# Performance work log

Measured on AMD Instinct MI355X. Metric: run time of the kernel, lower is better.

Reference implementation:

```python
import jax, jax.numpy as jnp
import numpy as np

N_CONST = 188
P = 16
HIDDEN = 128
DE = 5
DO = 6
N_TARGETS = 5
BATCH = 32


def _edge_indices(n):
    # receiver/sender pairs in the same order as itertools.product, skipping diagonal
    r, s = np.meshgrid(np.arange(n), np.arange(n), indexing='ij')
    mask = r != s
    return jnp.asarray(r[mask]), jnp.asarray(s[mask])  # each [n*(n-1)]


def _linear_params(key, fan_in, fan_out):
    kw, kb = jax.random.split(key)
    w = jax.random.normal(kw, (fan_in, fan_out), jnp.float32) / np.sqrt(fan_in)
    b = jax.random.normal(kb, (fan_out,), jnp.float32) * 0.01
    return w, b


def setup_inputs() -> dict:
    key = jax.random.key(0)
    ks = jax.random.split(key, 10)
    inp = {"x": jax.random.normal(ks[0], (BATCH, N_CONST, P), jnp.float32)}
    h2 = HIDDEN // 2
    dims = [
        ("fr1", 2 * P, HIDDEN), ("fr2", HIDDEN, h2), ("fr3", h2, DE),
        ("fo1", P + DE, HIDDEN), ("fo2", HIDDEN, h2), ("fo3", h2, DO),
        ("fc1", DO * N_CONST, HIDDEN), ("fc2", HIDDEN, h2), ("fc3", h2, N_TARGETS),
    ]
    for i, (name, fi, fo) in enumerate(dims):
        w, b = _linear_params(ks[i + 1], fi, fo)
        inp[name + "_w"] = w
        inp[name + "_b"] = b
    return inp


def reference(x, fr1_w, fr1_b, fr2_w, fr2_b, fr3_w, fr3_b,
              fo1_w, fo1_b, fo2_w, fo2_b, fo3_w, fo3_b,
              fc1_w, fc1_b, fc2_w, fc2_b, fc3_w, fc3_b):
    B, n, p = x.shape
    recv, send = _edge_indices(n)  # [Nr]
    # gather receiver/sender node features (replaces one-hot matmuls with Rr, Rs)
    e_in = jnp.concatenate([x[:, recv], x[:, send]], axis=-1)  # [B, Nr, 2P]
    h = jax.nn.relu(e_in @ fr1_w + fr1_b)
    h = jax.nn.relu(h @ fr2_w + fr2_b)
    E = jax.nn.relu(h @ fr3_w + fr3_b)  # [B, Nr, De]
    # scatter-add edge effects back to receiver nodes (replaces E @ Rr^T)
    Ebar = jnp.zeros((B, n, E.shape[-1]), x.dtype).at[:, recv].add(E)  # [B, N, De]
    c = jnp.concatenate([x, Ebar], axis=-1)  # [B, N, P+De]
    h = jax.nn.relu(c @ fo1_w + fo1_b)
    h = jax.nn.relu(h @ fo2_w + fo2_b)
    O = jax.nn.relu(h @ fo3_w + fo3_b)  # [B, N, Do]
    h = jax.nn.relu(O.reshape(B, -1) @ fc1_w + fc1_b)
    h = jax.nn.relu(h @ fc2_w + fc2_b)
    return h @ fc3_w + fc3_b  # [B, n_targets]
```

## Files before the change

### kernel.cpp

```cpp
#include <hip/hip_runtime.h>

#define BB   32
#define NN   188
#define PP   16
#define HID  128
#define HH2  64
#define DE   5
#define DO   6
#define NT   5
#define ROWS_O (BB*NN)
#define RT   32
#define KO   (PP+DE)

typedef __attribute__((ext_vector_type(8))) short short8;
typedef __attribute__((ext_vector_type(4))) float float4_;
typedef __attribute__((ext_vector_type(4))) unsigned uint4_;

__device__ __forceinline__ short f2bf(float v) {
    union { float f; unsigned u; } a; a.f = v;
    unsigned r = a.u + 0x7fff + ((a.u >> 16) & 1);
    return (short)(r >> 16);
}
__device__ __forceinline__ unsigned r2u(float v) {
    v = v > 0.f ? v : 0.f;
    return __float_as_uint(v) + 0x8000u;
}
__device__ __forceinline__ unsigned pack_hi16(unsigned hi, unsigned lo) {
    return __builtin_amdgcn_perm(hi, lo, 0x07060302);
}

#define XB_OFF    0
#define XB_ELTS   (BB*NN*24)
#define W1T_OFF   (XB_OFF + XB_ELTS)
#define W1T_ELTS  (HID*40)
#define W2S_OFF   (W1T_OFF + W1T_ELTS)
#define W2S_ELTS  (16*64*8)
#define W3S_OFF   (W2S_OFF + W2S_ELTS)
#define W3S_ELTS  (2*64*8)
#define SHORT_TOTAL (W3S_OFF + W3S_ELTS)

__device__ __forceinline__ int kmap(int q, int e) {
    return (e < 4) ? (q*4 + e) : (16 + q*4 + (e - 4));
}

__global__ void prep_kernel(const float* __restrict__ x,
                            const float* __restrict__ w1,
                            const float* __restrict__ w2,
                            const float* __restrict__ w3,
                            short* __restrict__ ws)
{
    const int i = blockIdx.x * blockDim.x + threadIdx.x;
    const int stride = gridDim.x * blockDim.x;
    for (int idx = i; idx < BB*NN*PP; idx += stride) {
        int row = idx >> 4, k = idx & 15;
        ws[XB_OFF + row*24 + k] = f2bf(x[idx]);
    }
    for (int idx = i; idx < 32*HID; idx += stride) {
        int k = idx >> 7, n = idx & 127;
        ws[W1T_OFF + n*40 + k] = f2bf(w1[idx]);
    }
    for (int idx = i; idx < W2S_ELTS; idx += stride) {
        int f = idx >> 9;
        int l = (idx >> 3) & 63;
        int e = idx & 7;
        int tt = f >> 2, s = f & 3;
        int q = l >> 4, n16 = l & 15;
        int k = 32*s + kmap(q, e);
        int n = tt*16 + n16;
        ws[W2S_OFF + idx] = f2bf(w2[k*HH2 + n]);
    }
    for (int idx = i; idx < W3S_ELTS; idx += stride) {
        int s2 = idx >> 9;
        int l = (idx >> 3) & 63;
        int e = idx & 7;
        int q = l >> 4, n16 = l & 15;
        int k = 32*s2 + kmap(q, e);
        ws[W3S_OFF + idx] = (n16 < DE) ? f2bf(w3[k*DE + n16]) : (short)0;
    }
}

__global__ __launch_bounds__(256)
void edge_mfma_kernel(const short* __restrict__ ws_s,
                      const float* __restrict__ b1,
                      const float* __restrict__ b2,
                      const float* __restrict__ b3,
                      float* __restrict__ ebar)
{
    const short* xb  = ws_s + XB_OFF;
    const short* w1t = ws_s + W1T_OFF;
    const short* w3g = ws_s + W3S_OFF;

    __shared__ __align__(16) unsigned wsmem[4096];
    __shared__ __align__(16) float sB1[HID];

    const int tid  = threadIdx.x;
    const int wave = tid >> 6;
    const int lane = tid & 63;
    const int n16  = lane & 15;
    const int q    = lane >> 4;
    const int bi   = blockIdx.x * 4 + wave;
    const int b    = bi / NN;
    const int recv = bi - b*NN;

    {
        const uint4* src = (const uint4*)(ws_s + W2S_OFF);
        uint4* dst = (uint4*)wsmem;
        #pragma unroll
        for (int i = 0; i < 4; ++i) dst[tid + i*256] = src[tid + i*256];
    }
    if (tid < HID) sB1[tid] = b1[tid];

    short8 W1f[8];
    #pragma unroll
    for (int t = 0; t < 8; ++t)
        W1f[t] = *(const short8*)(w1t + (t*16 + n16)*40 + q*8);
    short8 W3f[2];
    #pragma unroll
    for (int s = 0; s < 2; ++s)
        W3f[s] = *(const short8*)(w3g + s*512 + lane*8);
    float4_ bias2v[4];
    #pragma unroll
    for (int tt = 0; tt < 4; ++tt)
        bias2v[tt] = *(const float4_*)(b2 + tt*16 + q*4);
    float4_ bias3r;
    #pragma unroll
    for (int rg = 0; rg < 4; ++rg) {
        int o = q*4 + rg;
        bias3r[rg] = (o < DE) ? b3[o] : 0.f;
    }

    __syncthreads();

    const short* w2l = (const short*)wsmem;
    const short* xrow = xb + b*(NN*24);
    const bool rside = (q < 2);

    float acc[4] = {0.f, 0.f, 0.f, 0.f};

    short8 E1;
    {
        int send0 = n16 + (n16 >= recv ? 1 : 0);
        const int node = rside ? recv : send0;
        E1 = *(const short8*)(xrow + node*24 + (q & 1)*8);
    }

    #pragma unroll 2
    for (int ti = 0; ti < 12; ++ti) {
        short8 E1c = E1;
        if (ti < 11) {
            int en = (ti+1)*16 + n16;
            int send = en + (en >= recv ? 1 : 0);
            if (send > NN-1) send = NN-1;
            const int node = rside ? recv : send;
            E1 = *(const short8*)(xrow + node*24 + (q & 1)*8);
        }

        float4_ C2[4];
        #pragma unroll
        for (int tt = 0; tt < 4; ++tt) C2[tt] = bias2v[tt];

        #pragma unroll
        for (int s = 0; s < 4; ++s) {
            float4_ cb0 = *(const float4_*)(sB1 + (2*s)*16   + q*4);
            float4_ cb1 = *(const float4_*)(sB1 + (2*s+1)*16 + q*4);
            float4_ Ca = __builtin_amdgcn_mfma_f32_16x16x32_bf16(W1f[2*s],   E1c, cb0, 0, 0, 0);
            float4_ Cb = __builtin_amdgcn_mfma_f32_16x16x32_bf16(W1f[2*s+1], E1c, cb1, 0, 0, 0);
            uint4_ dv = (uint4_){ pack_hi16(r2u(Ca[1]), r2u(Ca[0])),
                                  pack_hi16(r2u(Ca[3]), r2u(Ca[2])),
                                  pack_hi16(r2u(Cb[1]), r2u(Cb[0])),
                                  pack_hi16(r2u(Cb[3]), r2u(Cb[2])) };
            short8 Bf = __builtin_bit_cast(short8, dv);
            #pragma unroll
            for (int tt = 0; tt < 4; ++tt) {
                short8 A2 = *(const short8*)(w2l + (tt*4 + s)*512 + lane*8);
                C2[tt] = __builtin_amdgcn_mfma_f32_16x16x32_bf16(A2, Bf, C2[tt], 0, 0, 0);
            }
        }

        float4_ C3 = bias3r;
        #pragma unroll
        for (int s2 = 0; s2 < 2; ++s2) {
            float4_ Cc = C2[2*s2], Cd = C2[2*s2+1];
            uint4_ dv = (uint4_){ pack_hi16(r2u(Cc[1]), r2u(Cc[0])),
                                  pack_hi16(r2u(Cc[3]), r2u(Cc[2])),
                                  pack_hi16(r2u(Cd[1]), r2u(Cd[0])),
                                  pack_hi16(r2u(Cd[3]), r2u(Cd[2])) };
            short8 B3f = __builtin_bit_cast(short8, dv);
            C3 = __builtin_amdgcn_mfma_f32_16x16x32_bf16(W3f[s2], B3f, C3, 0, 0, 0);
        }
        const int e = ti*16 + n16;
        const bool ok = (e < NN-1);
        #pragma unroll
        for (int rg = 0; rg < 4; ++rg) {
            float v = C3[rg];
            v = v > 0.f ? v : 0.f;
            acc[rg] += ok ? v : 0.f;
        }
    }

    #pragma unroll
    for (int rg = 0; rg < 4; ++rg) {
        acc[rg] += __shfl_xor(acc[rg], 1);
        acc[rg] += __shfl_xor(acc[rg], 2);
        acc[rg] += __shfl_xor(acc[rg], 4);
        acc[rg] += __shfl_xor(acc[rg], 8);
    }
    if (n16 == 0) {
        #pragma unroll
        for (int rg = 0; rg < 4; ++rg) {
            int o = q*4 + rg;
            if (o < DE) ebar[bi*DE + o] = acc[rg];
        }
    }
}

__global__ __launch_bounds__(512)
void obj_mlp_kernel(const float* __restrict__ x, const float* __restrict__ ebar,
                    const float* __restrict__ w1, const float* __restrict__ b1,
                    const float* __restrict__ w2, const float* __restrict__ b2,
                    const float* __restrict__ w3, const float* __restrict__ b3,
                    float* __restrict__ o_out)
{
    __shared__ float sW[HID*HH2];
    __shared__ float sB1[HID];
    __shared__ float sB2[HH2];
    __shared__ float sCin[RT*KO];
    __shared__ float sH1[RT*HID];
    __shared__ float sH2t[HH2*(RT+1)];
    const int tid = threadIdx.x;
    const int rbase = blockIdx.x * RT;

    for (int i = tid; i < KO*HID; i += 512) sW[i] = w1[i];
    if (tid < HID) sB1[tid] = b1[tid];
    else if (tid < HID+HH2) sB2[tid-HID] = b2[tid-HID];
    for (int i = tid; i < RT*KO; i += 512) {
        int r = i / KO, k = i - r*KO;
        int gr = rbase + r;
        int b = gr / NN;
        int node = gr - b*NN;
        sCin[i] = (k < PP) ? x[(b*NN+node)*PP + k]
                           : ebar[(b*NN+node)*DE + (k-PP)];
    }
    __syncthreads();

    {
        const int j = tid & (HID-1);
        const int g = tid >> 7;
        float w[KO];
        #pragma unroll
        for (int k = 0; k < KO; ++k) w[k] = sW[k*HID + j];
        const float bj = sB1[j];
        #pragma unroll
        for (int rr = 0; rr < 8; ++rr) {
            const int r = g*8 + rr;
            const float* e = &sCin[r*KO];
            float a0=0.f,a1=0.f,a2=0.f;
            #pragma unroll
            for (int k = 0; k < KO; k += 3) {
                a0 += w[k+0]*e[k+0];
                a1 += w[k+1]*e[k+1];
                a2 += w[k+2]*e[k+2];
            }
            float v = a0+a1+a2+bj;
            sH1[r*HID + j] = v > 0.f ? v : 0.f;
        }
    }
    __syncthreads();
    for (int i = tid; i < HID*HH2; i += 512) sW[i] = w2[i];
    __syncthreads();

    {
        const int j = tid & (HH2-1);
        const int g = tid >> 6;
        float acc[4];
        #pragma unroll
        for (int rr = 0; rr < 4; ++rr) acc[rr] = sB2[j];
        #pragma unroll
        for (int kc = 0; kc < HID; kc += 32) {
            float w[32];
            #pragma unroll
            for (int kk = 0; kk < 32; ++kk) w[kk] = sW[(kc+kk)*HH2 + j];
            #pragma unroll
            for (int rr = 0; rr < 4; ++rr) {
                const float* h = &sH1[(g*4+rr)*HID + kc];
                float a0=0.f,a1=0.f,a2=0.f,a3=0.f;
                #pragma unroll
                for (int kk = 0; kk < 32; kk += 4) {
                    a0 += w[kk+0]*h[kk+0];
                    a1 += w[kk+1]*h[kk+1];
                    a2 += w[kk+2]*h[kk+2];
                    a3 += w[kk+3]*h[kk+3];
                }
                acc[rr] += (a0+a1)+(a2+a3);
            }
        }
        #pragma unroll
        for (int rr = 0; rr < 4; ++rr) {
            float v = acc[rr];
            sH2t[j*(RT+1) + (g*4+rr)] = v > 0.f ? v : 0.f;
        }
    }
    __syncthreads();

    if (tid < RT*DO) {
        const int r = tid & (RT-1);
        const int c = tid >> 5;
        float a0=0.f,a1=0.f,a2=0.f,a3=0.f;
        #pragma unroll
        for (int k = 0; k < HH2; k += 4) {
            a0 += sH2t[(k+0)*(RT+1)+r]*w3[(k+0)*DO+c];
            a1 += sH2t[(k+1)*(RT+1)+r]*w3[(k+1)*DO+c];
            a2 += sH2t[(k+2)*(RT+1)+r]*w3[(k+2)*DO+c];
            a3 += sH2t[(k+3)*(RT+1)+r]*w3[(k+3)*DO+c];
        }
        float v = (a0+a1)+(a2+a3) + b3[c];
        v = v > 0.f ? v : 0.f;
        int gr = rbase + r;
        int b = gr / NN;
        int node = gr - b*NN;
        o_out[b*(NN*DO) + node*DO + c] = v;
    }
}

__global__ __launch_bounds__(256)
void fc_kernel(const float* __restrict__ o_in,
               const float* __restrict__ w1, const float* __restrict__ b1,
               const float* __restrict__ w2, const float* __restrict__ b2,
               const float* __restrict__ w3, const float* __restrict__ b3,
               float* __restrict__ out)
{
    __shared__ __align__(16) float s_in[NN*DO];
    __shared__ float s_p[256];
    __shared__ float s_h1[HID];
    __shared__ float s_h2[HH2];
    const int b = blockIdx.x, tid = threadIdx.x;

    for (int i = tid; i < NN*DO; i += 256) s_in[i] = o_in[b*(NN*DO) + i];
    __syncthreads();

    {
        const int j = tid & (HID-1);
        const int h = tid >> 7;
        const float4* s4 = (const float4*)&s_in[h*564];
        const float* wbase = w1 + (size_t)(h*564)*HID + j;
        float a0=0.f,a1=0.f,a2=0.f,a3=0.f;
        #pragma unroll 4
        for (int i = 0; i < 141; ++i) {
            float4 v = s4[i];
            const float* wp = wbase + (size_t)i*4*HID;
            a0 += v.x * wp[0];
            a1 += v.y * wp[HID];
            a2 += v.z * wp[2*HID];
            a3 += v.w * wp[3*HID];
        }
        s_p[tid] = (a0+a1)+(a2+a3);
    }
    __syncthreads();
    if (tid < HID) {
        float v = s_p[tid] + s_p[tid+HID] + b1[tid];
        s_h1[tid] = v > 0.f ? v : 0.f;
    }
    __syncthreads();

    {
        const int j = tid & (HH2-1);
        const int q = tid >> 6;
        float acc = 0.f;
        #pragma unroll
        for (int kk = 0; kk < 32; ++kk) {
            int k = q*32 + kk;
            acc += s_h1[k] * w2[k*HH2 + j];
        }
        s_p[tid] = acc;
    }
    __syncthreads();
    if (tid < HH2) {
        float v = s_p[tid] + s_p[tid+64] + s_p[tid+128] + s_p[tid+192] + b2[tid];
        s_h2[tid] = v > 0.f ? v : 0.f;
    }
    __syncthreads();

    if (tid < NT) {
        float acc = b3[tid];
        #pragma unroll
        for (int k = 0; k < HH2; ++k)
            acc += s_h2[k] * w3[k*NT + tid];
        out[b*NT + tid] = acc;
    }
}

extern "C" void kernel_launch(void* const* d_in, const int* in_sizes, int n_in,
                              void* d_out, int out_size, void* d_ws, size_t ws_size,
                              hipStream_t stream) {
    (void)in_sizes; (void)n_in; (void)out_size; (void)ws_size;
    const float* x     = (const float*)d_in[0];
    const float* fr1_w = (const float*)d_in[1];
    const float* fr1_b = (const float*)d_in[2];
    const float* fr2_w = (const float*)d_in[3];
    const float* fr2_b = (const float*)d_in[4];
    const float* fr3_w = (const float*)d_in[5];
    const float* fr3_b = (const float*)d_in[6];
    const float* fo1_w = (const float*)d_in[7];
    const float* fo1_b = (const float*)d_in[8];
    const float* fo2_w = (const float*)d_in[9];
    const float* fo2_b = (const float*)d_in[10];
    const float* fo3_w = (const float*)d_in[11];
    const float* fo3_b = (const float*)d_in[12];
    const float* fc1_w = (const float*)d_in[13];
    const float* fc1_b = (const float*)d_in[14];
    const float* fc2_w = (const float*)d_in[15];
    const float* fc2_b = (const float*)d_in[16];
    const float* fc3_w = (const float*)d_in[17];
    const float* fc3_b = (const float*)d_in[18];

    short* ws_s = (short*)d_ws;
    size_t fbase = ((size_t)SHORT_TOTAL*2 + 15) & ~(size_t)15;
    float* ebar = (float*)((char*)d_ws + fbase);
    float* o_ws = ebar + BB*NN*DE;

    prep_kernel<<<128, 256, 0, stream>>>(x, fr1_w, fr2_w, fr3_w, ws_s);
    edge_mfma_kernel<<<(BB*NN)/4, 256, 0, stream>>>(ws_s, fr1_b, fr2_b, fr3_b, ebar);
    obj_mlp_kernel<<<ROWS_O/RT, 512, 0, stream>>>(
        x, ebar, fo1_w, fo1_b, fo2_w, fo2_b, fo3_w, fo3_b, o_ws);
    fc_kernel<<<BB, 256, 0, stream>>>(
        o_ws, fc1_w, fc1_b, fc2_w, fc2_b, fc3_w, fc3_b, (float*)d_out);
}
```

Baseline: 171.7 us.

## Move W1 fragments and bias2 to LDS, use hardware bf16 pack, raise occupancy

```diff
diff --git a/kernel.cpp b/kernel.cpp
--- a/kernel.cpp
+++ b/kernel.cpp
@@ -21,12 +21,12 @@
     unsigned r = a.u + 0x7fff + ((a.u >> 16) & 1);
     return (short)(r >> 16);
 }
-__device__ __forceinline__ unsigned r2u(float v) {
-    v = v > 0.f ? v : 0.f;
-    return __float_as_uint(v) + 0x8000u;
-}
-__device__ __forceinline__ unsigned pack_hi16(unsigned hi, unsigned lo) {
-    return __builtin_amdgcn_perm(hi, lo, 0x07060302);
+__device__ __forceinline__ unsigned relu_pk(float lo, float hi) {
+    float l = lo > 0.f ? lo : 0.f;
+    float h = hi > 0.f ? hi : 0.f;
+    unsigned r;
+    asm("v_cvt_pk_bf16_f32 %0, %1, %2" : "=v"(r) : "v"(l), "v"(h));
+    return r;
 }
 
 #define XB_OFF    0
@@ -79,7 +79,7 @@
     }
 }
 
-__global__ __launch_bounds__(256)
+__global__ __launch_bounds__(256, 6)
 void edge_mfma_kernel(const short* __restrict__ ws_s,
                       const float* __restrict__ b1,
                       const float* __restrict__ b2,
@@ -91,7 +91,9 @@
     const short* w3g = ws_s + W3S_OFF;
 
     __shared__ __align__(16) unsigned wsmem[4096];
+    __shared__ __align__(16) short sW1[8*64*8];
     __shared__ __align__(16) float sB1[HID];
+    __shared__ __align__(16) float sB2[HH2];
 
     const int tid  = threadIdx.x;
     const int wave = tid >> 6;
@@ -108,20 +110,21 @@
         #pragma unroll
         for (int i = 0; i < 4; ++i) dst[tid + i*256] = src[tid + i*256];
     }
+    #pragma unroll
+    for (int i = 0; i < 2; ++i) {
+        int f  = tid + i*256;
+        int t  = f >> 6, l = f & 63;
+        int qq = l >> 4, nn = l & 15;
+        uint4 v = *(const uint4*)(w1t + (t*16 + nn)*40 + qq*8);
+        *((uint4*)sW1 + f) = v;
+    }
     if (tid < HID) sB1[tid] = b1[tid];
-
-    short8 W1f[8];
-    #pragma unroll
-    for (int t = 0; t < 8; ++t)
-        W1f[t] = *(const short8*)(w1t + (t*16 + n16)*40 + q*8);
+    else if (tid < HID + HH2) sB2[tid - HID] = b2[tid - HID];
+
     short8 W3f[2];
     #pragma unroll
     for (int s = 0; s < 2; ++s)
         W3f[s] = *(const short8*)(w3g + s*512 + lane*8);
-    float4_ bias2v[4];
-    #pragma unroll
-    for (int tt = 0; tt < 4; ++tt)
-        bias2v[tt] = *(const float4_*)(b2 + tt*16 + q*4);
     float4_ bias3r;
     #pragma unroll
     for (int rg = 0; rg < 4; ++rg) {
@@ -132,6 +135,7 @@
     __syncthreads();
 
     const short* w2l = (const short*)wsmem;
+    const short8* w1l = (const short8*)sW1;
     const short* xrow = xb + b*(NN*24);
     const bool rside = (q < 2);
 
@@ -144,7 +148,7 @@
         E1 = *(const short8*)(xrow + node*24 + (q & 1)*8);
     }
 
-    #pragma unroll 2
+    #pragma unroll 1
     for (int ti = 0; ti < 12; ++ti) {
         short8 E1c = E1;
         if (ti < 11) {
@@ -157,18 +161,21 @@
 
         float4_ C2[4];
         #pragma unroll
-        for (int tt = 0; tt < 4; ++tt) C2[tt] = bias2v[tt];
+        for (int tt = 0; tt < 4; ++tt)
+            C2[tt] = *(const float4_*)(sB2 + tt*16 + q*4);
 
         #pragma unroll
         for (int s = 0; s < 4; ++s) {
             float4_ cb0 = *(const float4_*)(sB1 + (2*s)*16   + q*4);
             float4_ cb1 = *(const float4_*)(sB1 + (2*s+1)*16 + q*4);
-            float4_ Ca = __builtin_amdgcn_mfma_f32_16x16x32_bf16(W1f[2*s],   E1c, cb0, 0, 0, 0);
-            float4_ Cb = __builtin_amdgcn_mfma_f32_16x16x32_bf16(W1f[2*s+1], E1c, cb1, 0, 0, 0);
-            uint4_ dv = (uint4_){ pack_hi16(r2u(Ca[1]), r2u(Ca[0])),
-                                  pack_hi16(r2u(Ca[3]), r2u(Ca[2])),
-                                  pack_hi16(r2u(Cb[1]), r2u(Cb[0])),
-                                  pack_hi16(r2u(Cb[3]), r2u(Cb[2])) };
+            short8 A1a = w1l[(2*s)*64   + lane];
+            short8 A1b = w1l[(2*s+1)*64 + lane];
+            float4_ Ca = __builtin_amdgcn_mfma_f32_16x16x32_bf16(A1a, E1c, cb0, 0, 0, 0);
+            float4_ Cb = __builtin_amdgcn_mfma_f32_16x16x32_bf16(A1b, E1c, cb1, 0, 0, 0);
+            uint4_ dv = (uint4_){ relu_pk(Ca[0], Ca[1]),
+                                  relu_pk(Ca[2], Ca[3]),
+                                  relu_pk(Cb[0], Cb[1]),
+                                  relu_pk(Cb[2], Cb[3]) };
             short8 Bf = __builtin_bit_cast(short8, dv);
             #pragma unroll
             for (int tt = 0; tt < 4; ++tt) {
@@ -181,10 +188,10 @@
         #pragma unroll
         for (int s2 = 0; s2 < 2; ++s2) {
             float4_ Cc = C2[2*s2], Cd = C2[2*s2+1];
-            uint4_ dv = (uint4_){ pack_hi16(r2u(Cc[1]), r2u(Cc[0])),
-                                  pack_hi16(r2u(Cc[3]), r2u(Cc[2])),
-                                  pack_hi16(r2u(Cd[1]), r2u(Cd[0])),
-                                  pack_hi16(r2u(Cd[3]), r2u(Cd[2])) };
+            uint4_ dv = (uint4_){ relu_pk(Cc[0], Cc[1]),
+                                  relu_pk(Cc[2], Cc[3]),
+                                  relu_pk(Cd[0], Cd[1]),
+                                  relu_pk(Cd[2], Cd[3]) };
             short8 B3f = __builtin_bit_cast(short8, dv);
             C3 = __builtin_amdgcn_mfma_f32_16x16x32_bf16(W3f[s2], B3f, C3, 0, 0, 0);
         }
```

After: 174.1 us. Within noise of the previous version (+1.4%).
